# Kernel tuning notes

Measured on AMD Instinct MI355X. Metric: run time of the kernel, lower is better.

The kernel has to match this reference:

```python
import jax, jax.numpy as jnp
import numpy as np

N_NODES = 50000
N_EDGES = 800000
H = 256
EDGE_DIM = 3
N_LAYERS = 3
MLP_LAYERS = 3


def setup_inputs() -> dict:
    key = jax.random.key(0)
    ks = jax.random.split(key, 16)
    s = 1.0 / np.sqrt(H)
    inp = {
        'x': jax.random.normal(ks[0], (N_NODES, H), dtype=jnp.float32),
        'edge_index': jax.random.randint(ks[1], (2, N_EDGES), 0, N_NODES, dtype=jnp.int64),
        'edge_attr': jax.random.normal(ks[2], (N_EDGES, EDGE_DIM), dtype=jnp.float32),
        # per-layer edge-attr projection Linear(3 -> H)
        'We': jax.random.normal(ks[3], (N_LAYERS, EDGE_DIM, H), dtype=jnp.float32) / np.sqrt(EDGE_DIM),
        'be': jax.random.normal(ks[4], (N_LAYERS, H), dtype=jnp.float32) * 0.01,
        # per-layer inner mlp: MLP_LAYERS linears of [H, H]
        'Wm': jax.random.normal(ks[5], (N_LAYERS, MLP_LAYERS, H, H), dtype=jnp.float32) * s,
        'bm': jax.random.normal(ks[6], (N_LAYERS, MLP_LAYERS, H), dtype=jnp.float32) * 0.01,
        # final projection head: Linear -> ReLU -> Linear
        'pW1': jax.random.normal(ks[7], (H, H), dtype=jnp.float32) * s,
        'pb1': jax.random.normal(ks[8], (H,), dtype=jnp.float32) * 0.01,
        'pW2': jax.random.normal(ks[9], (H, H), dtype=jnp.float32) * s,
        'pb2': jax.random.normal(ks[10], (H,), dtype=jnp.float32) * 0.01,
    }
    return inp


def _inner_mlp(h, Wl, bl):
    # mlp.forward: linear, relu between layers, no relu after last
    for i in range(MLP_LAYERS):
        h = h @ Wl[i] + bl[i]
        if i < MLP_LAYERS - 1:
            h = jax.nn.relu(h)
    return h


def reference(x, edge_index, edge_attr, We, be, Wm, bm, pW1, pb1, pW2, pb2):
    src = edge_index[0]  # x_j (source / message sender)
    dst = edge_index[1]  # x_i (destination / aggregation target)
    for l in range(N_LAYERS):
        x0 = x
        # GINEConv: msg = ReLU(x_j + lin_edge(edge_attr)); sum-agg at dst; eps=0
        e = edge_attr @ We[l] + be[l]                      # [E, H]
        msg = jax.nn.relu(x[src] + e)                      # [E, H] edge gather
        agg = jax.ops.segment_sum(msg, dst, num_segments=N_NODES)  # scatter-sum
        h = _inner_mlp(x + agg, Wm[l], bm[l])              # (1+eps)*x + agg, eps=0
        x = jax.nn.relu(h) + x0                            # residual in gin.forward
    # proj head: Linear -> ReLU -> Linear
    out = jax.nn.relu(x @ pW1 + pb1) @ pW2 + pb2
    return out
```

## Files before the change

### kernel.cpp

```cpp
#include <hip/hip_runtime.h>

#define NNODES 50000
#define NEDGES 800000
#define HD 256
#define NSB 196
#define BM 64
#define BUFB (BM * 512)

typedef __attribute__((ext_vector_type(8))) short bf16x8;
typedef __attribute__((ext_vector_type(4))) float f32x4;

__device__ __forceinline__ unsigned int f2bf(float f) {
    union { float f; unsigned int u; } v; v.f = f;
    unsigned int u = v.u;
    u += 0x7fffu + ((u >> 16) & 1u);
    return u >> 16;
}
__device__ __forceinline__ float b2f(unsigned short u) {
    union { unsigned int u; float f; } v; v.u = ((unsigned int)u) << 16;
    return v.f;
}

__global__ __launch_bounds__(256) void prep_all(
    const float* __restrict__ x, unsigned short* __restrict__ xb,
    const float* __restrict__ Wm, const float* __restrict__ pW1,
    const float* __restrict__ pW2, unsigned short* __restrict__ Wpk,
    int* __restrict__ deg) {
    int i = blockIdx.x * 256 + threadIdx.x;
    if (i < 3200000) {
        float4 v = reinterpret_cast<const float4*>(x)[i];
        ushort4 o;
        o.x = (unsigned short)f2bf(v.x);
        o.y = (unsigned short)f2bf(v.y);
        o.z = (unsigned short)f2bf(v.z);
        o.w = (unsigned short)f2bf(v.w);
        reinterpret_cast<ushort4*>(xb)[i] = o;
    } else if (i < 3200000 + 11 * 65536) {
        int g = i - 3200000;
        int mat = g >> 16;
        int r = g & 65535;
        int j = r & 7, lane = (r >> 3) & 63, kb = (r >> 9) & 7, ct = r >> 12;
        int k = kb * 32 + ((lane >> 4) << 3) + j;
        int c = ct * 16 + (lane & 15);
        const float* s = (mat < 9) ? (Wm + (size_t)mat * 65536)
                                   : ((mat == 9) ? pW1 : pW2);
        Wpk[g] = (unsigned short)f2bf(s[k * 256 + c]);
    } else if (i < 3200000 + 11 * 65536 + NNODES) {
        deg[i - 3200000 - 11 * 65536] = 0;
    }
}

__global__ __launch_bounds__(256) void hist_kernel(const int* __restrict__ dst,
                                                   int* __restrict__ deg) {
    int e = blockIdx.x * 256 + threadIdx.x;
    if (e < NEDGES) atomicAdd(&deg[dst[e]], 1);
}

__global__ __launch_bounds__(256) void scan_part(const int* __restrict__ deg,
                                                 int* __restrict__ bsum) {
    __shared__ int red[256];
    int t = threadIdx.x;
    int i = blockIdx.x * 256 + t;
    red[t] = (i < NNODES) ? deg[i] : 0;
    __syncthreads();
    for (int off = 128; off > 0; off >>= 1) {
        if (t < off) red[t] += red[t + off];
        __syncthreads();
    }
    if (t == 0) bsum[blockIdx.x] = red[0];
}

__global__ __launch_bounds__(256) void scan_fin(const int* __restrict__ deg,
                                                const int* __restrict__ bsum,
                                                int* __restrict__ rowptr,
                                                int* __restrict__ cursor) {
    __shared__ int sb[256];
    __shared__ int s[256];
    int t = threadIdx.x;
    int bv = (t < NSB) ? bsum[t] : 0;
    sb[t] = bv;
    __syncthreads();
    for (int off = 1; off < 256; off <<= 1) {
        int u = (t >= off) ? sb[t - off] : 0;
        __syncthreads();
        sb[t] += u;
        __syncthreads();
    }
    int i = blockIdx.x * 256 + t;
    int v = (i < NNODES) ? deg[i] : 0;
    s[t] = v;
    __syncthreads();
    for (int off = 1; off < 256; off <<= 1) {
        int u = (t >= off) ? s[t - off] : 0;
        __syncthreads();
        s[t] += u;
        __syncthreads();
    }
    int base = (blockIdx.x == 0) ? 0 : sb[blockIdx.x - 1];
    int val = base + s[t] - v;
    if (i < NNODES) {
        rowptr[i] = val;
        cursor[i] = val;
    }
    if (i == NNODES) rowptr[i] = val;
}

__global__ __launch_bounds__(256) void fill_csr(const int* __restrict__ src,
                                                const int* __restrict__ dst,
                                                const float* __restrict__ ea,
                                                int* __restrict__ cursor,
                                                int4* __restrict__ epack) {
    int e = blockIdx.x * 256 + threadIdx.x;
    if (e >= NEDGES) return;
    int pos = atomicAdd(&cursor[dst[e]], 1);
    int4 v;
    v.x = src[e] * HD;
    v.y = __float_as_int(ea[e * 3 + 0]);
    v.z = __float_as_int(ea[e * 3 + 1]);
    v.w = __float_as_int(ea[e * 3 + 2]);
    epack[pos] = v;
}

__global__ __launch_bounds__(256) void agg_kernel(
    const unsigned short* __restrict__ xb, const int* __restrict__ rowptr,
    const int4* __restrict__ epack, const float* __restrict__ We,
    const float* __restrict__ be, unsigned short* __restrict__ out) {
    const int wave = threadIdx.x >> 6;
    const int lane = threadIdx.x & 63;
    const int n = blockIdx.x * 4 + wave;
    const int c = lane * 4;
    const float4 w0 = *reinterpret_cast<const float4*>(We + c);
    const float4 w1 = *reinterpret_cast<const float4*>(We + HD + c);
    const float4 w2 = *reinterpret_cast<const float4*>(We + 2 * HD + c);
    const float4 bb = *reinterpret_cast<const float4*>(be + c);
    const unsigned short* xbc = xb + c;
    ushort4 xv = *reinterpret_cast<const ushort4*>(xbc + (size_t)n * HD);
    float4 acc = make_float4(b2f(xv.x), b2f(xv.y), b2f(xv.z), b2f(xv.w));
    const int beg = __builtin_amdgcn_readfirstlane(rowptr[n]);
    const int end = __builtin_amdgcn_readfirstlane(rowptr[n + 1]);

#define EDGE_ACC(E, XS)                                                              \
    {                                                                                \
        float a0 = __int_as_float((E).y);                                            \
        float a1 = __int_as_float((E).z);                                            \
        float a2 = __int_as_float((E).w);                                            \
        acc.x += fmaxf(fmaf(a0, w0.x, fmaf(a1, w1.x, fmaf(a2, w2.x,                  \
                       b2f((XS).x) + bb.x))), 0.f);                                  \
        acc.y += fmaxf(fmaf(a0, w0.y, fmaf(a1, w1.y, fmaf(a2, w2.y,                  \
                       b2f((XS).y) + bb.y))), 0.f);                                  \
        acc.z += fmaxf(fmaf(a0, w0.z, fmaf(a1, w1.z, fmaf(a2, w2.z,                  \
                       b2f((XS).z) + bb.z))), 0.f);                                  \
        acc.w += fmaxf(fmaf(a0, w0.w, fmaf(a1, w1.w, fmaf(a2, w2.w,                  \
                       b2f((XS).w) + bb.w))), 0.f);                                  \
    }

    int i = beg;
    for (; i + 4 <= end; i += 4) {
        int4 e0 = epack[i];
        int4 e1 = epack[i + 1];
        int4 e2 = epack[i + 2];
        int4 e3 = epack[i + 3];
        ushort4 s0 = *reinterpret_cast<const ushort4*>(xbc + e0.x);
        ushort4 s1 = *reinterpret_cast<const ushort4*>(xbc + e1.x);
        ushort4 s2 = *reinterpret_cast<const ushort4*>(xbc + e2.x);
        ushort4 s3 = *reinterpret_cast<const ushort4*>(xbc + e3.x);
        EDGE_ACC(e0, s0);
        EDGE_ACC(e1, s1);
        EDGE_ACC(e2, s2);
        EDGE_ACC(e3, s3);
    }
    for (; i < end; ++i) {
        int4 e0 = epack[i];
        ushort4 s0 = *reinterpret_cast<const ushort4*>(xbc + e0.x);
        EDGE_ACC(e0, s0);
    }
#undef EDGE_ACC

    ushort4 o;
    o.x = (unsigned short)f2bf(acc.x);
    o.y = (unsigned short)f2bf(acc.y);
    o.z = (unsigned short)f2bf(acc.z);
    o.w = (unsigned short)f2bf(acc.w);
    *reinterpret_cast<ushort4*>(out + (size_t)n * HD + c) = o;
}

__device__ __forceinline__ void load_b(const unsigned short* __restrict__ Wp,
                                       int wave, int lane, int kb, bf16x8* dst) {
#pragma unroll
    for (int ct = 0; ct < 2; ++ct)
        dst[ct] = *reinterpret_cast<const bf16x8*>(
            Wp + ((size_t)(((wave * 2 + ct) * 8 + kb) * 64 + lane)) * 8);
}

template <int NPH, int RES_PH, bool RELU_LAST, bool OUTF32>
__global__ __launch_bounds__(512, 4) void gemm_fused(
    const unsigned short* __restrict__ A, const unsigned short* __restrict__ Wpk,
    const float* __restrict__ b0, const float* __restrict__ b1,
    const float* __restrict__ b2, const float* __restrict__ b3,
    const float* __restrict__ b4, const unsigned short* __restrict__ res,
    void* __restrict__ outv) {
    __shared__ __align__(16) unsigned char lds[2 * BUFB];
    const int tid = threadIdx.x;
    const int rbase = blockIdx.x * BM;
    const int wave = tid >> 6;
    const int lane = tid & 63;
    const int lr = lane & 15;
    const int lg = lane >> 4;

    bf16x8 bb[3][2];
    load_b(Wpk, wave, lane, 0, bb[0]);
    load_b(Wpk, wave, lane, 1, bb[1]);

    {
        const unsigned char* Ab = (const unsigned char*)A;
#pragma unroll
        for (int it = 0; it < 4; ++it) {
            int r0 = wave * 8 + it * 2;
            int row = r0 + (lane >> 5);
            int cb = (lane & 31) * 16;
            int grow = rbase + row;
            if (grow >= NNODES) grow = NNODES - 1;
            const unsigned char* src =
                Ab + (size_t)grow * 512 + (cb ^ ((row & 7) << 4));
            __builtin_amdgcn_global_load_lds(
                (const __attribute__((address_space(1))) void*)src,
                (__attribute__((address_space(3))) void*)(lds + r0 * 512), 16, 0, 0);
        }
    }
    __syncthreads();

#pragma unroll
    for (int ph = 0; ph < NPH; ++ph) {
        const unsigned short* Wp = Wpk + (size_t)ph * 65536;
        const float* bias = (ph == 0) ? b0
                          : (ph == 1) ? b1
                          : (ph == 2) ? b2
                          : (ph == 3) ? b3 : b4;
        unsigned char* rbuf = lds + (ph & 1) * BUFB;
        unsigned char* wbuf = lds + ((ph & 1) ^ 1) * BUFB;

        f32x4 acc[4][2];
#pragma unroll
        for (int rt = 0; rt < 4; ++rt)
#pragma unroll
            for (int ct = 0; ct < 2; ++ct) acc[rt][ct] = (f32x4){0.f, 0.f, 0.f, 0.f};

#pragma unroll
        for (int kb = 0; kb < 8; ++kb) {
            if (kb + 2 < 8) load_b(Wp, wave, lane, kb + 2, bb[(kb + 2) % 3]);
            const int kbyte = kb * 64 + lg * 16;
#pragma unroll
            for (int rt = 0; rt < 4; ++rt) {
                int row = rt * 16 + lr;
                int off = row * 512 + (kbyte ^ ((row & 7) << 4));
                bf16x8 a = *reinterpret_cast<const bf16x8*>(rbuf + off);
#pragma unroll
                for (int ct = 0; ct < 2; ++ct)
                    acc[rt][ct] = __builtin_amdgcn_mfma_f32_16x16x32_bf16(
                        a, bb[kb % 3][ct], acc[rt][ct], 0, 0, 0);
            }
        }

        if (ph < NPH - 1) {
#pragma unroll
            for (int rt = 0; rt < 4; ++rt) {
#pragma unroll
                for (int ct = 0; ct < 2; ++ct) {
                    int c = wave * 32 + ct * 16 + lr;
                    float bv = bias[c];
#pragma unroll
                    for (int i = 0; i < 4; ++i) {
                        int row = rt * 16 + lg * 4 + i;
                        float v = fmaxf(acc[rt][ct][i] + bv, 0.f);
                        if (ph == RES_PH)
                            v += b2f(res[(size_t)(rbase + row) * HD + c]);
                        int off = row * 512 + ((2 * c) ^ ((row & 7) << 4));
                        *reinterpret_cast<unsigned short*>(wbuf + off) =
                            (unsigned short)f2bf(v);
                    }
                }
            }
            const unsigned short* Wn = Wpk + (size_t)(ph + 1) * 65536;
            load_b(Wn, wave, lane, 0, bb[0]);
            load_b(Wn, wave, lane, 1, bb[1]);
            __syncthreads();
        } else {
#pragma unroll
            for (int rt = 0; rt < 4; ++rt) {
                int row0 = rbase + rt * 16 + lg * 4;
#pragma unroll
                for (int ct = 0; ct < 2; ++ct) {
                    int c = wave * 32 + ct * 16 + lr;
                    float bv = bias[c];
#pragma unroll
                    for (int i = 0; i < 4; ++i) {
                        int row = row0 + i;
                        if (row < NNODES) {
                            float v = acc[rt][ct][i] + bv;
                            if (RELU_LAST) v = fmaxf(v, 0.f);
                            if (RES_PH == NPH - 1)
                                v += b2f(res[(size_t)row * HD + c]);
                            if (OUTF32)
                                reinterpret_cast<float*>(outv)[(size_t)row * HD + c] = v;
                            else
                                reinterpret_cast<unsigned short*>(
                                    outv)[(size_t)row * HD + c] =
                                    (unsigned short)f2bf(v);
                        }
                    }
                }
            }
        }
    }
}

extern "C" void kernel_launch(void* const* d_in, const int* in_sizes, int n_in,
                              void* d_out, int out_size, void* d_ws, size_t ws_size,
                              hipStream_t stream) {
    const float* x   = (const float*)d_in[0];
    const int*   ei  = (const int*)d_in[1];
    const float* ea  = (const float*)d_in[2];
    const float* We  = (const float*)d_in[3];
    const float* be  = (const float*)d_in[4];
    const float* Wm  = (const float*)d_in[5];
    const float* bm  = (const float*)d_in[6];
    const float* pW1 = (const float*)d_in[7];
    const float* pb1 = (const float*)d_in[8];
    const float* pW2 = (const float*)d_in[9];
    const float* pb2 = (const float*)d_in[10];
    float* out = (float*)d_out;

    const size_t NH = (size_t)NNODES * HD;
    unsigned short* xb   = (unsigned short*)d_ws;
    unsigned short* curb = xb + NH;
    unsigned short* aggb = curb + NH;
    unsigned short* Wpk  = aggb + NH;
    int* rowptr = (int*)(Wpk + 11 * 65536);
    int* cursor = rowptr + 50004;
    int* deg    = cursor + 50004;
    int* bsum   = deg + 50004;
    int4* epack = (int4*)d_out;

    const int* srcI = ei;
    const int* dstI = ei + NEDGES;

    const int prep_threads = 3200000 + 11 * 65536 + NNODES;
    prep_all<<<dim3((prep_threads + 255) / 256), dim3(256), 0, stream>>>(
        x, xb, Wm, pW1, pW2, Wpk, deg);
    hist_kernel<<<dim3((NEDGES + 255) / 256), dim3(256), 0, stream>>>(dstI, deg);
    scan_part<<<dim3(NSB), dim3(256), 0, stream>>>(deg, bsum);
    scan_fin<<<dim3(NSB), dim3(256), 0, stream>>>(deg, bsum, rowptr, cursor);
    fill_csr<<<dim3((NEDGES + 255) / 256), dim3(256), 0, stream>>>(srcI, dstI, ea,
                                                                   cursor, epack);

    const int gemm_grid = (NNODES + BM - 1) / BM;
    for (int l = 0; l < 2; ++l) {
        const unsigned short* xin = (l == 0) ? xb : curb;
        agg_kernel<<<dim3(NNODES / 4), dim3(256), 0, stream>>>(
            xin, rowptr, epack, We + (size_t)l * 3 * HD, be + (size_t)l * HD, aggb);
        gemm_fused<3, 2, true, false><<<dim3(gemm_grid), dim3(512), 0, stream>>>(
            aggb, Wpk + (size_t)l * 3 * 65536, bm + (size_t)(l * 3 + 0) * HD,
            bm + (size_t)(l * 3 + 1) * HD, bm + (size_t)(l * 3 + 2) * HD,
            nullptr, nullptr, xin, curb);
    }
    agg_kernel<<<dim3(NNODES / 4), dim3(256), 0, stream>>>(
        curb, rowptr, epack, We + (size_t)2 * 3 * HD, be + (size_t)2 * HD, aggb);
    gemm_fused<5, 2, false, true><<<dim3(gemm_grid), dim3(512), 0, stream>>>(
        aggb, Wpk + (size_t)6 * 65536, bm + (size_t)6 * HD, bm + (size_t)7 * HD,
        bm + (size_t)8 * HD, pb1, pb2, curb, out);
}
```

Measured before the change: 424.1 us.

## Fuse edge aggregation into the per-layer MLP GEMM kernel for first two layers

Adds a layer_fused kernel that gathers and sums each block's 64 node messages straight into LDS (in the swizzled bf16 layout), then runs the three-layer MLP with MFMA from LDS. The first two GIN layers use it, which drops the separate agg kernel launch and the global write and read of the aggregate buffer. Each block now does the irregular gather across 8 waves of 8 nodes before any MFMA work. That can lower memory-latency hiding compared with the standalone agg kernel, which ran 12500 small blocks, and it leaves less room to overlap gather with compute. Buffers are rotated so the last layer still uses the separate agg and gemm kernels.

```diff
diff --git a/kernel.cpp b/kernel.cpp
--- a/kernel.cpp
+++ b/kernel.cpp
@@ -121,39 +121,29 @@
     epack[pos] = v;
 }
 
-__global__ __launch_bounds__(256) void agg_kernel(
-    const unsigned short* __restrict__ xb, const int* __restrict__ rowptr,
-    const int4* __restrict__ epack, const float* __restrict__ We,
-    const float* __restrict__ be, unsigned short* __restrict__ out) {
-    const int wave = threadIdx.x >> 6;
-    const int lane = threadIdx.x & 63;
-    const int n = blockIdx.x * 4 + wave;
-    const int c = lane * 4;
-    const float4 w0 = *reinterpret_cast<const float4*>(We + c);
-    const float4 w1 = *reinterpret_cast<const float4*>(We + HD + c);
-    const float4 w2 = *reinterpret_cast<const float4*>(We + 2 * HD + c);
-    const float4 bb = *reinterpret_cast<const float4*>(be + c);
-    const unsigned short* xbc = xb + c;
-    ushort4 xv = *reinterpret_cast<const ushort4*>(xbc + (size_t)n * HD);
-    float4 acc = make_float4(b2f(xv.x), b2f(xv.y), b2f(xv.z), b2f(xv.w));
-    const int beg = __builtin_amdgcn_readfirstlane(rowptr[n]);
-    const int end = __builtin_amdgcn_readfirstlane(rowptr[n + 1]);
-
 #define EDGE_ACC(E, XS)                                                              \
     {                                                                                \
         float a0 = __int_as_float((E).y);                                            \
         float a1 = __int_as_float((E).z);                                            \
         float a2 = __int_as_float((E).w);                                            \
         acc.x += fmaxf(fmaf(a0, w0.x, fmaf(a1, w1.x, fmaf(a2, w2.x,                  \
-                       b2f((XS).x) + bb.x))), 0.f);                                  \
+                       b2f((XS).x) + bbv.x))), 0.f);                                 \
         acc.y += fmaxf(fmaf(a0, w0.y, fmaf(a1, w1.y, fmaf(a2, w2.y,                  \
-                       b2f((XS).y) + bb.y))), 0.f);                                  \
+                       b2f((XS).y) + bbv.y))), 0.f);                                 \
         acc.z += fmaxf(fmaf(a0, w0.z, fmaf(a1, w1.z, fmaf(a2, w2.z,                  \
-                       b2f((XS).z) + bb.z))), 0.f);                                  \
+                       b2f((XS).z) + bbv.z))), 0.f);                                 \
         acc.w += fmaxf(fmaf(a0, w0.w, fmaf(a1, w1.w, fmaf(a2, w2.w,                  \
-                       b2f((XS).w) + bb.w))), 0.f);                                  \
-    }
-
+                       b2f((XS).w) + bbv.w))), 0.f);                                 \
+    }
+
+__device__ __forceinline__ float4 gather_node(
+    const unsigned short* __restrict__ xbc, const int* __restrict__ rowptr,
+    const int4* __restrict__ epack, int nc, float4 w0, float4 w1, float4 w2,
+    float4 bbv) {
+    ushort4 xv = *reinterpret_cast<const ushort4*>(xbc + (size_t)nc * HD);
+    float4 acc = make_float4(b2f(xv.x), b2f(xv.y), b2f(xv.z), b2f(xv.w));
+    const int beg = __builtin_amdgcn_readfirstlane(rowptr[nc]);
+    const int end = __builtin_amdgcn_readfirstlane(rowptr[nc + 1]);
     int i = beg;
     for (; i + 4 <= end; i += 4) {
         int4 e0 = epack[i];
@@ -174,8 +164,22 @@
         ushort4 s0 = *reinterpret_cast<const ushort4*>(xbc + e0.x);
         EDGE_ACC(e0, s0);
     }
-#undef EDGE_ACC
-
+    return acc;
+}
+
+__global__ __launch_bounds__(256) void agg_kernel(
+    const unsigned short* __restrict__ xb, const int* __restrict__ rowptr,
+    const int4* __restrict__ epack, const float* __restrict__ We,
+    const float* __restrict__ be, unsigned short* __restrict__ out) {
+    const int wave = threadIdx.x >> 6;
+    const int lane = threadIdx.x & 63;
+    const int n = blockIdx.x * 4 + wave;
+    const int c = lane * 4;
+    const float4 w0 = *reinterpret_cast<const float4*>(We + c);
+    const float4 w1 = *reinterpret_cast<const float4*>(We + HD + c);
+    const float4 w2 = *reinterpret_cast<const float4*>(We + 2 * HD + c);
+    const float4 bbv = *reinterpret_cast<const float4*>(be + c);
+    float4 acc = gather_node(xb + c, rowptr, epack, n, w0, w1, w2, bbv);
     ushort4 o;
     o.x = (unsigned short)f2bf(acc.x);
     o.y = (unsigned short)f2bf(acc.y);
@@ -190,6 +194,120 @@
     for (int ct = 0; ct < 2; ++ct)
         dst[ct] = *reinterpret_cast<const bf16x8*>(
             Wp + ((size_t)(((wave * 2 + ct) * 8 + kb) * 64 + lane)) * 8);
+}
+
+__global__ __launch_bounds__(512, 4) void layer_fused(
+    const unsigned short* __restrict__ xb, const int* __restrict__ rowptr,
+    const int4* __restrict__ epack, const float* __restrict__ We,
+    const float* __restrict__ be, const unsigned short* __restrict__ Wpk,
+    const float* __restrict__ b0, const float* __restrict__ b1,
+    const float* __restrict__ b2, unsigned short* __restrict__ outb) {
+    __shared__ __align__(16) unsigned char lds[2 * BUFB];
+    const int tid = threadIdx.x;
+    const int rbase = blockIdx.x * BM;
+    const int wave = tid >> 6;
+    const int lane = tid & 63;
+    const int lr = lane & 15;
+    const int lg = lane >> 4;
+    const int c = lane * 4;
+
+    {
+        const float4 w0 = *reinterpret_cast<const float4*>(We + c);
+        const float4 w1 = *reinterpret_cast<const float4*>(We + HD + c);
+        const float4 w2 = *reinterpret_cast<const float4*>(We + 2 * HD + c);
+        const float4 bbv = *reinterpret_cast<const float4*>(be + c);
+        const unsigned short* xbc = xb + c;
+        for (int j = 0; j < 8; ++j) {
+            int row = wave * 8 + j;
+            int n = rbase + row;
+            int nc = (n < NNODES) ? n : (NNODES - 1);
+            float4 acc = gather_node(xbc, rowptr, epack, nc, w0, w1, w2, bbv);
+            ushort4 o;
+            o.x = (unsigned short)f2bf(acc.x);
+            o.y = (unsigned short)f2bf(acc.y);
+            o.z = (unsigned short)f2bf(acc.z);
+            o.w = (unsigned short)f2bf(acc.w);
+            int off = row * 512 + ((lane * 8) ^ ((row & 7) << 4));
+            *reinterpret_cast<ushort4*>(lds + off) = o;
+        }
+    }
+
+    bf16x8 bb[3][2];
+    load_b(Wpk, wave, lane, 0, bb[0]);
+    load_b(Wpk, wave, lane, 1, bb[1]);
+    __syncthreads();
+
+#pragma unroll
+    for (int ph = 0; ph < 3; ++ph) {
+        const unsigned short* Wp = Wpk + (size_t)ph * 65536;
+        const float* bias = (ph == 0) ? b0 : ((ph == 1) ? b1 : b2);
+        unsigned char* rbuf = lds + (ph & 1) * BUFB;
+        unsigned char* wbuf = lds + ((ph & 1) ^ 1) * BUFB;
+
+        f32x4 acc[4][2];
+#pragma unroll
+        for (int rt = 0; rt < 4; ++rt)
+#pragma unroll
+            for (int ct = 0; ct < 2; ++ct) acc[rt][ct] = (f32x4){0.f, 0.f, 0.f, 0.f};
+
+#pragma unroll
+        for (int kb = 0; kb < 8; ++kb) {
+            if (kb + 2 < 8) load_b(Wp, wave, lane, kb + 2, bb[(kb + 2) % 3]);
+            const int kbyte = kb * 64 + lg * 16;
+#pragma unroll
+            for (int rt = 0; rt < 4; ++rt) {
+                int row = rt * 16 + lr;
+                int off = row * 512 + (kbyte ^ ((row & 7) << 4));
+                bf16x8 a = *reinterpret_cast<const bf16x8*>(rbuf + off);
+#pragma unroll
+                for (int ct = 0; ct < 2; ++ct)
+                    acc[rt][ct] = __builtin_amdgcn_mfma_f32_16x16x32_bf16(
+                        a, bb[kb % 3][ct], acc[rt][ct], 0, 0, 0);
+            }
+        }
+
+        if (ph < 2) {
+#pragma unroll
+            for (int rt = 0; rt < 4; ++rt) {
+#pragma unroll
+                for (int ct = 0; ct < 2; ++ct) {
+                    int cc = wave * 32 + ct * 16 + lr;
+                    float bv = bias[cc];
+#pragma unroll
+                    for (int i = 0; i < 4; ++i) {
+                        int row = rt * 16 + lg * 4 + i;
+                        float v = fmaxf(acc[rt][ct][i] + bv, 0.f);
+                        int off = row * 512 + ((2 * cc) ^ ((row & 7) << 4));
+                        *reinterpret_cast<unsigned short*>(wbuf + off) =
+                            (unsigned short)f2bf(v);
+                    }
+                }
+            }
+            const unsigned short* Wn = Wpk + (size_t)(ph + 1) * 65536;
+            load_b(Wn, wave, lane, 0, bb[0]);
+            load_b(Wn, wave, lane, 1, bb[1]);
+            __syncthreads();
+        } else {
+#pragma unroll
+            for (int rt = 0; rt < 4; ++rt) {
+                int row0 = rbase + rt * 16 + lg * 4;
+#pragma unroll
+                for (int ct = 0; ct < 2; ++ct) {
+                    int cc = wave * 32 + ct * 16 + lr;
+                    float bv = bias[cc];
+#pragma unroll
+                    for (int i = 0; i < 4; ++i) {
+                        int row = row0 + i;
+                        if (row < NNODES) {
+                            float v = fmaxf(acc[rt][ct][i] + bv, 0.f);
+                            v += b2f(xb[(size_t)row * HD + cc]);
+                            outb[(size_t)row * HD + cc] = (unsigned short)f2bf(v);
+                        }
+                    }
+                }
+            }
+        }
+    }
 }
 
 template <int NPH, int RES_PH, bool RELU_LAST, bool OUTF32>
@@ -266,15 +384,15 @@
             for (int rt = 0; rt < 4; ++rt) {
 #pragma unroll
                 for (int ct = 0; ct < 2; ++ct) {
-                    int c = wave * 32 + ct * 16 + lr;
-                    float bv = bias[c];
+                    int cc = wave * 32 + ct * 16 + lr;
+                    float bv = bias[cc];
 #pragma unroll
                     for (int i = 0; i < 4; ++i) {
                         int row = rt * 16 + lg * 4 + i;
                         float v = fmaxf(acc[rt][ct][i] + bv, 0.f);
                         if (ph == RES_PH)
-                            v += b2f(res[(size_t)(rbase + row) * HD + c]);
-                        int off = row * 512 + ((2 * c) ^ ((row & 7) << 4));
+                            v += b2f(res[(size_t)(rbase + row) * HD + cc]);
+                        int off = row * 512 + ((2 * cc) ^ ((row & 7) << 4));
                         *reinterpret_cast<unsigned short*>(wbuf + off) =
                             (unsigned short)f2bf(v);
                     }
@@ -290,8 +408,8 @@
                 int row0 = rbase + rt * 16 + lg * 4;
 #pragma unroll
                 for (int ct = 0; ct < 2; ++ct) {
-                    int c = wave * 32 + ct * 16 + lr;
-                    float bv = bias[c];
+                    int cc = wave * 32 + ct * 16 + lr;
+                    float bv = bias[cc];
 #pragma unroll
                     for (int i = 0; i < 4; ++i) {
                         int row = row0 + i;
@@ -299,12 +417,12 @@
                             float v = acc[rt][ct][i] + bv;
                             if (RELU_LAST) v = fmaxf(v, 0.f);
                             if (RES_PH == NPH - 1)
-                                v += b2f(res[(size_t)row * HD + c]);
+                                v += b2f(res[(size_t)row * HD + cc]);
                             if (OUTF32)
-                                reinterpret_cast<float*>(outv)[(size_t)row * HD + c] = v;
+                                reinterpret_cast<float*>(outv)[(size_t)row * HD + cc] = v;
                             else
                                 reinterpret_cast<unsigned short*>(
-                                    outv)[(size_t)row * HD + c] =
+                                    outv)[(size_t)row * HD + cc] =
                                     (unsigned short)f2bf(v);
                         }
                     }
@@ -353,19 +471,15 @@
     fill_csr<<<dim3((NEDGES + 255) / 256), dim3(256), 0, stream>>>(srcI, dstI, ea,
                                                                    cursor, epack);
 
-    const int gemm_grid = (NNODES + BM - 1) / BM;
-    for (int l = 0; l < 2; ++l) {
-        const unsigned short* xin = (l == 0) ? xb : curb;
-        agg_kernel<<<dim3(NNODES / 4), dim3(256), 0, stream>>>(
-            xin, rowptr, epack, We + (size_t)l * 3 * HD, be + (size_t)l * HD, aggb);
-        gemm_fused<3, 2, true, false><<<dim3(gemm_grid), dim3(512), 0, stream>>>(
-            aggb, Wpk + (size_t)l * 3 * 65536, bm + (size_t)(l * 3 + 0) * HD,
-            bm + (size_t)(l * 3 + 1) * HD, bm + (size_t)(l * 3 + 2) * HD,
-            nullptr, nullptr, xin, curb);
-    }
+    const int grid = (NNODES + BM - 1) / BM;
+    layer_fused<<<dim3(grid), dim3(512), 0, stream>>>(
+        xb, rowptr, epack, We, be, Wpk, bm, bm + HD, bm + 2 * HD, curb);
+    layer_fused<<<dim3(grid), dim3(512), 0, stream>>>(
+        curb, rowptr, epack, We + 3 * HD, be + HD, Wpk + (size_t)3 * 65536,
+        bm + 3 * HD, bm + 4 * HD, bm + 5 * HD, aggb);
     agg_kernel<<<dim3(NNODES / 4), dim3(256), 0, stream>>>(
-        curb, rowptr, epack, We + (size_t)2 * 3 * HD, be + (size_t)2 * HD, aggb);
-    gemm_fused<5, 2, false, true><<<dim3(gemm_grid), dim3(512), 0, stream>>>(
-        aggb, Wpk + (size_t)6 * 65536, bm + (size_t)6 * HD, bm + (size_t)7 * HD,
-        bm + (size_t)8 * HD, pb1, pb2, curb, out);
-}
+        aggb, rowptr, epack, We + 6 * HD, be + 2 * HD, curb);
+    gemm_fused<5, 2, false, true><<<dim3(grid), dim3(512), 0, stream>>>(
+        curb, Wpk + (size_t)6 * 65536, bm + 6 * HD, bm + 7 * HD, bm + 8 * HD,
+        pb1, pb2, aggb, out);
+}
```

Measured after the change: 444.0 us. 1.05x slower.
